# Performance work log

Hardware: AMD Instinct MI355X
Metric: run time of the kernel (lower is better)

## Reference

```python
import math
import jax, jax.numpy as jnp
import numpy as np

B, S, HID = 2, 2048, 3072
NH, HD = 32, 96            # num_heads, head_dim; num_kv_heads == num_heads (n_rep = 1)
OP = NH * HD + 2 * (NH * HD)  # 9216


def _rope_tables(seq_len, head_dim, theta=10000.0):
    inv_freq = 1.0 / (theta ** (np.arange(0, head_dim, 2, dtype=np.float32) / head_dim))
    t = np.arange(seq_len, dtype=np.float32)
    freqs = np.outer(t, inv_freq)                      # [S, HD/2]
    emb = np.concatenate([freqs, freqs], axis=-1)      # [S, HD]
    return jnp.asarray(np.cos(emb)), jnp.asarray(np.sin(emb))


def setup_inputs() -> dict:
    key = jax.random.key(0)
    k1, k2, k3 = jax.random.split(key, 3)
    hidden_states = jax.random.normal(k1, (B, S, HID), dtype=jnp.float32)
    cos, sin = _rope_tables(S, HD)
    # additive causal mask [B, 1, S, S]
    neg = jnp.finfo(jnp.float32).min
    causal = jnp.where(jnp.tril(jnp.ones((S, S), dtype=bool)), 0.0, neg)
    attention_mask = jnp.broadcast_to(causal[None, None], (B, 1, S, S)).astype(jnp.float32)
    Wqkv = jax.random.normal(k2, (HID, OP), dtype=jnp.float32) * (HID ** -0.5)
    Wo = jax.random.normal(k3, (NH * HD, HID), dtype=jnp.float32) * ((NH * HD) ** -0.5)
    return {"hidden_states": hidden_states, "cos": cos, "sin": sin,
            "attention_mask": attention_mask, "Wqkv": Wqkv, "Wo": Wo}


def _rotate_half(x):
    x1, x2 = jnp.split(x, 2, axis=-1)
    return jnp.concatenate([-x2, x1], axis=-1)


def reference(hidden_states, cos, sin, attention_mask, Wqkv, Wo):
    bsz, q_len, _ = hidden_states.shape
    qkv = hidden_states @ Wqkv                                    # [B,S,OP]
    q, k, v = jnp.split(qkv, [NH * HD, 2 * NH * HD], axis=-1)
    # [B,S,H*D] -> [B,H,S,D]
    to_bhsd = lambda t: t.reshape(bsz, q_len, NH, HD).transpose(0, 2, 1, 3)
    q, k, v = to_bhsd(q), to_bhsd(k), to_bhsd(v)
    c = cos[None, None]                                           # [1,1,S,D]
    s = sin[None, None]
    q = q * c + _rotate_half(q) * s
    k = k * c + _rotate_half(k) * s
    # num_key_value_groups == 1, so repeat_kv is identity.
    scores = jnp.einsum('bhqd,bhkd->bhqk', q, k) / math.sqrt(HD)  # [B,H,S,S]
    scores = scores + attention_mask
    attn = jax.nn.softmax(scores.astype(jnp.float32), axis=-1).astype(v.dtype)
    # dropout p=0.0 / eval -> identity
    out = jnp.einsum('bhqk,bhkd->bhqd', attn, v)                  # [B,H,S,D]
    out = out.transpose(0, 2, 1, 3).reshape(bsz, q_len, NH * HD)
    return out @ Wo                                               # [B,S,HID]
```

## Files before the change

kernel.cpp:

```cpp
#include <hip/hip_runtime.h>

typedef __bf16  bf16x8 __attribute__((ext_vector_type(8)));
typedef float   f32x4  __attribute__((ext_vector_type(4)));
typedef float   f32x16 __attribute__((ext_vector_type(16)));
typedef short   i16x8  __attribute__((ext_vector_type(8)));
typedef unsigned short u16x4 __attribute__((ext_vector_type(4)));
typedef unsigned int   u32x4 __attribute__((ext_vector_type(4)));

__device__ __forceinline__ float bf2f(unsigned short u) {
    union { unsigned int i; float f; } v; v.i = ((unsigned int)u) << 16; return v.f;
}
__device__ __forceinline__ unsigned short f2bf(float f) {
    union { float f; unsigned int i; } v; v.f = f;
    unsigned int r = v.i + 0x7FFFu + ((v.i >> 16) & 1u);
    return (unsigned short)(r >> 16);
}
__device__ __forceinline__ unsigned pk2(float lo, float hi) {
    union { __bf16 h[2]; unsigned u; } t;
    t.h[0] = (__bf16)lo; t.h[1] = (__bf16)hi;
    return t.u;
}
__device__ __forceinline__ unsigned short cvt1(float x) {
    union { __bf16 h; unsigned short u; } t;
    t.h = (__bf16)x;
    return t.u;
}
__device__ __forceinline__ void gload_lds16(const void* g, void* l) {
    __builtin_amdgcn_global_load_lds(
        (const __attribute__((address_space(1))) void*)g,
        (__attribute__((address_space(3))) void*)l, 16, 0, 0);
}
__device__ __forceinline__ void pswap(unsigned &x, unsigned &y) {
#if __has_builtin(__builtin_amdgcn_permlane32_swap)
    auto r = __builtin_amdgcn_permlane32_swap((int)x, (int)y, false, false);
    x = (unsigned)r[0]; y = (unsigned)r[1];
#else
    unsigned nx = (threadIdx.x & 32) ? (unsigned)__shfl_xor((int)y, 32) : x;
    unsigned ny = (threadIdx.x & 32) ? y : (unsigned)__shfl_xor((int)x, 32);
    x = nx; y = ny;
#endif
}
__device__ __forceinline__ float partner_f(float v, int hi) {
    unsigned x = __builtin_bit_cast(unsigned, v), y = x;
    pswap(x, y);
    return __builtin_bit_cast(float, hi ? x : y);
}

__global__ __launch_bounds__(256) void cast_f32_bf16(
    const float* __restrict__ in, unsigned short* __restrict__ out, int n8)
{
    int i = blockIdx.x * 256 + threadIdx.x;
    if (i >= n8) return;
    const f32x4* p = (const f32x4*)(in + (long)i * 8);
    f32x4 a = p[0], b = p[1];
    i16x8 o;
    o[0]=(short)f2bf(a[0]); o[1]=(short)f2bf(a[1]); o[2]=(short)f2bf(a[2]); o[3]=(short)f2bf(a[3]);
    o[4]=(short)f2bf(b[0]); o[5]=(short)f2bf(b[1]); o[6]=(short)f2bf(b[2]); o[7]=(short)f2bf(b[3]);
    *(i16x8*)(out + (long)i * 8) = o;
}

__global__ __launch_bounds__(256) void transpose_cast(
    const float* __restrict__ in, unsigned short* __restrict__ out, int R, int C)
{
    __shared__ float tile[64][65];
    int c0 = blockIdx.x * 64, r0 = blockIdx.y * 64;
    int tx = threadIdx.x & 63, ty = threadIdx.x >> 6;
#pragma unroll
    for (int i = 0; i < 64; i += 4)
        tile[ty + i][tx] = in[(long)(r0 + ty + i) * C + c0 + tx];
    __syncthreads();
#pragma unroll
    for (int i = 0; i < 64; i += 4)
        out[(long)(c0 + ty + i) * R + r0 + tx] = f2bf(tile[tx][ty + i]);
}

template <int MODE>
__global__ __launch_bounds__(256) void gemm_bt(
    const unsigned short* __restrict__ A, const unsigned short* __restrict__ B,
    int K, int N,
    unsigned short* __restrict__ Qo, unsigned short* __restrict__ Ko,
    unsigned short* __restrict__ Vo, float* __restrict__ Cf)
{
    __shared__ unsigned short Al[128 * 64];
    __shared__ unsigned short Bl[128 * 64];
    const int t = threadIdx.x;
    const int w = t >> 6, l = t & 63, lhi = l >> 4, llo = l & 15;
    const int m0 = blockIdx.x * 128, n0 = blockIdx.y * 128;
    const int wmo = (w >> 1) << 6, wno = (w & 1) << 6;

    const unsigned short* ag[4];
    const unsigned short* bg[4];
#pragma unroll
    for (int i = 0; i < 4; ++i) {
        int j = i * 256 + t;
        int row = j >> 3;
        int c = (j & 7) ^ (row & 7);
        ag[i] = A + (long)(m0 + row) * K + c * 8;
        bg[i] = B + (long)(n0 + row) * K + c * 8;
    }

    f32x4 acc[4][4] = {};
    const int nkt = K >> 6;
    for (int kt = 0; kt < nkt; ++kt) {
        __syncthreads();
#pragma unroll
        for (int i = 0; i < 4; ++i) {
            gload_lds16(ag[i] + kt * 64, &Al[(i * 256 + (w << 6)) * 8]);
            gload_lds16(bg[i] + kt * 64, &Bl[(i * 256 + (w << 6)) * 8]);
        }
        __syncthreads();
#pragma unroll
        for (int kf = 0; kf < 2; ++kf) {
            bf16x8 af[4], bfv[4];
#pragma unroll
            for (int mi = 0; mi < 4; ++mi) {
                int row = wmo + mi * 16 + llo;
                int cc = (kf * 4 + lhi) ^ (row & 7);
                af[mi] = __builtin_bit_cast(bf16x8, *(const i16x8*)&Al[row * 64 + cc * 8]);
            }
#pragma unroll
            for (int ni = 0; ni < 4; ++ni) {
                int row = wno + ni * 16 + llo;
                int cc = (kf * 4 + lhi) ^ (row & 7);
                bfv[ni] = __builtin_bit_cast(bf16x8, *(const i16x8*)&Bl[row * 64 + cc * 8]);
            }
#pragma unroll
            for (int mi = 0; mi < 4; ++mi)
#pragma unroll
                for (int ni = 0; ni < 4; ++ni)
                    acc[mi][ni] = __builtin_amdgcn_mfma_f32_16x16x32_bf16(
                        af[mi], bfv[ni], acc[mi][ni], 0, 0, 0);
        }
    }

#pragma unroll
    for (int mi = 0; mi < 4; ++mi) {
        int s0g = m0 + wmo + mi * 16 + (lhi << 2);
#pragma unroll
        for (int ni = 0; ni < 4; ++ni) {
            int gcol = n0 + wno + ni * 16 + llo;
            if (MODE == 1) {
#pragma unroll
                for (int r = 0; r < 4; ++r)
                    Cf[(long)(s0g + r) * N + gcol] = acc[mi][ni][r];
            } else {
                int seg = gcol / 3072;
                int cc2 = gcol - seg * 3072;
                int h = cc2 / 96, d = cc2 - h * 96;
                int b = s0g >> 11, s = s0g & 2047;
                long bh = (long)((b << 5) + h);
                if (seg == 2) {
                    u16x4 pv;
#pragma unroll
                    for (int r = 0; r < 4; ++r) pv[r] = f2bf(acc[mi][ni][r]);
                    *(u16x4*)(Vo + (bh * 96 + d) * 2048 + s) = pv;
                } else {
                    unsigned short* dst = seg ? Ko : Qo;
#pragma unroll
                    for (int r = 0; r < 4; ++r)
                        dst[(bh * 2048 + s + r) * 96 + d] = f2bf(acc[mi][ni][r]);
                }
            }
        }
    }
}

__global__ __launch_bounds__(256) void rope_kernel(
    unsigned short* __restrict__ Qb, unsigned short* __restrict__ Kb,
    const float* __restrict__ cosT, const float* __restrict__ sinT)
{
    int i = blockIdx.x * 256 + threadIdx.x;
    int d6 = i % 6;
    int sbh = i / 6;
    int s = sbh & 2047;
    long base = (long)sbh * 96 + d6 * 8;
    const f32x4* cp = (const f32x4*)(cosT + s * 96 + d6 * 8);
    const f32x4* sp = (const f32x4*)(sinT + s * 96 + d6 * 8);
    f32x4 c0 = cp[0], c1 = cp[1], s0 = sp[0], s1 = sp[1];
    float cv[8] = {c0[0],c0[1],c0[2],c0[3],c1[0],c1[1],c1[2],c1[3]};
    float sv[8] = {s0[0],s0[1],s0[2],s0[3],s1[0],s1[1],s1[2],s1[3]};
    i16x8 qlo = *(i16x8*)(Qb + base), qhi = *(i16x8*)(Qb + base + 48);
    i16x8 klo = *(i16x8*)(Kb + base), khi = *(i16x8*)(Kb + base + 48);
    i16x8 qlo2, qhi2, klo2, khi2;
#pragma unroll
    for (int j = 0; j < 8; ++j) {
        float ql = bf2f((unsigned short)qlo[j]), qh = bf2f((unsigned short)qhi[j]);
        float kl = bf2f((unsigned short)klo[j]), kh = bf2f((unsigned short)khi[j]);
        qlo2[j] = (short)f2bf(ql * cv[j] - qh * sv[j]);
        qhi2[j] = (short)f2bf(qh * cv[j] + ql * sv[j]);
        klo2[j] = (short)f2bf(kl * cv[j] - kh * sv[j]);
        khi2[j] = (short)f2bf(kh * cv[j] + kl * sv[j]);
    }
    *(i16x8*)(Qb + base) = qlo2; *(i16x8*)(Qb + base + 48) = qhi2;
    *(i16x8*)(Kb + base) = klo2; *(i16x8*)(Kb + base + 48) = khi2;
}

__global__ __launch_bounds__(256, 2) void attn_fwd(
    const unsigned short* __restrict__ Q, const unsigned short* __restrict__ Kt,
    const unsigned short* __restrict__ Vg, unsigned short* __restrict__ O)
{
    __shared__ __align__(16) unsigned short Kl[2][64 * 128];
    __shared__ __align__(16) unsigned short Vl[2][96 * 64];
    const int t = threadIdx.x;
    const int w = t >> 6, l = t & 63;
    const int l31 = l & 31, hi = l >> 5, l7 = l & 7;
    const int bh = blockIdx.x;
    constexpr float C2 = 0.14724450f;

    const unsigned short* Kg  = Kt + (long)bh * 2048 * 96;
    const unsigned short* Vgb = Vg + (long)bh * 96 * 2048;

#define STAGE_KV(buf, tile)                                                        \
    {                                                                              \
        _Pragma("unroll")                                                          \
        for (int i_ = 0; i_ < 4; ++i_) {                                           \
            int row_ = (w << 4) + (i_ << 2) + (l >> 4);                            \
            gload_lds16(Kg + ((long)(tile) * 64 + row_) * 96 +                     \
                            (((l & 15) ^ (row_ & 7)) << 3),                        \
                        &Kl[buf][((w << 4) + (i_ << 2)) << 7]);                    \
        }                                                                          \
        _Pragma("unroll")                                                          \
        for (int i_ = 0; i_ < 3; ++i_) {                                           \
            int row_ = w * 24 + (i_ << 3) + (l >> 3);                              \
            gload_lds16(Vgb + (long)row_ * 2048 + (tile) * 64 +                    \
                            ((l7 ^ (row_ & 7)) << 3),                              \
                        &Vl[buf][(w * 24 + (i_ << 3)) << 6]);                      \
        }                                                                          \
    }

    const int b = bh >> 5, h = bh & 31;

    for (int pass = 0; pass < 2; ++pass) {
        const int qt = pass ? 15 - (int)blockIdx.y : (int)blockIdx.y;
        const int q0b = qt << 7;
        const int nkv = 2 * qt + 2;
        const int kd  = 2 * qt + (w >> 1);

        bf16x8 qf[6];
        {
            const unsigned short* qp =
                Q + ((long)bh * 2048 + q0b + (w << 5) + l31) * 96 + (hi << 3);
#pragma unroll
            for (int ks = 0; ks < 6; ++ks)
                qf[ks] = __builtin_bit_cast(bf16x8, *(const i16x8*)(qp + ks * 16));
        }

        f32x16 oa[3] = {};
        float m_r = -1e30f, l_r = 0.f;

        STAGE_KV(0, 0);
        STAGE_KV(1, 1);

        for (int kt = 0; kt < nkv; ++kt) {
            const int cb = kt & 1;
            if (kt < nkv - 1) asm volatile("s_waitcnt vmcnt(7)" ::: "memory");
            else              asm volatile("s_waitcnt vmcnt(0)" ::: "memory");
            __builtin_amdgcn_s_barrier();

            if (kt <= kd) {
                f32x16 s0 = {}, s1 = {};
                __builtin_amdgcn_s_setprio(1);
#pragma unroll
                for (int ks = 0; ks < 6; ++ks) {
                    bf16x8 k0 = __builtin_bit_cast(bf16x8, *(const i16x8*)
                        &Kl[cb][(l31 << 7) + ((((ks << 1) + hi) ^ l7) << 3)]);
                    bf16x8 k1 = __builtin_bit_cast(bf16x8, *(const i16x8*)
                        &Kl[cb][((32 + l31) << 7) + ((((ks << 1) + hi) ^ l7) << 3)]);
                    s0 = __builtin_amdgcn_mfma_f32_32x32x16_bf16(k0, qf[ks], s0, 0, 0, 0);
                    s1 = __builtin_amdgcn_mfma_f32_32x32x16_bf16(k1, qf[ks], s1, 0, 0, 0);
                }
                __builtin_amdgcn_s_setprio(0);

                if (kt == kd) {
#pragma unroll
                    for (int r = 0; r < 16; ++r) {
                        int kvl = (r & 3) + ((r >> 2) << 3) + (hi << 2);
                        if (w & 1) {
                            if (kvl > l31) s1[r] = -1e30f;
                        } else {
                            if (kvl > l31) s0[r] = -1e30f;
                            s1[r] = -1e30f;
                        }
                    }
                }
                float px = s0[0];
#pragma unroll
                for (int r = 1; r < 16; ++r) px = fmaxf(px, s0[r]);
#pragma unroll
                for (int r = 0; r < 16; ++r) px = fmaxf(px, s1[r]);
                px = fmaxf(px, partner_f(px, hi));
                if (__any(px > m_r + 54.0f)) {
                    float mnew = fmaxf(m_r, px);
                    float scl = exp2f((m_r - mnew) * C2);
                    l_r *= scl;
#pragma unroll
                    for (int tt = 0; tt < 3; ++tt)
#pragma unroll
                        for (int r = 0; r < 16; ++r) oa[tt][r] *= scl;
                    m_r = mnew;
                }
                const float mC = m_r * C2;
                float ls = 0.f;
#pragma unroll
                for (int r = 0; r < 16; ++r) {
                    s0[r] = exp2f(fmaf(s0[r], C2, -mC));
                    s1[r] = exp2f(fmaf(s1[r], C2, -mC));
                    ls += s0[r] + s1[r];
                }
                l_r += ls;
                bf16x8 pf[4];
#pragma unroll
                for (int s = 0; s < 4; ++s) {
                    const f32x16& pv = (s >= 2) ? s1 : s0;
                    const int bb = (s & 1) << 3;
                    unsigned d0 = pk2(pv[bb + 0], pv[bb + 1]);
                    unsigned d2 = pk2(pv[bb + 4], pv[bb + 5]);
                    pswap(d0, d2);
                    unsigned d1 = pk2(pv[bb + 2], pv[bb + 3]);
                    unsigned d3 = pk2(pv[bb + 6], pv[bb + 7]);
                    pswap(d1, d3);
                    pf[s] = __builtin_bit_cast(bf16x8, (u32x4){d0, d1, d2, d3});
                }
                __builtin_amdgcn_s_setprio(1);
#pragma unroll
                for (int s = 0; s < 4; ++s) {
#pragma unroll
                    for (int tt = 0; tt < 3; ++tt) {
                        bf16x8 vf = __builtin_bit_cast(bf16x8, *(const i16x8*)
                            &Vl[cb][((tt << 5) + l31) * 64 + ((((s << 1) + hi) ^ l7) << 3)]);
                        oa[tt] = __builtin_amdgcn_mfma_f32_32x32x16_bf16(vf, pf[s], oa[tt], 0, 0, 0);
                    }
                }
                __builtin_amdgcn_s_setprio(0);
            }

            asm volatile("s_waitcnt lgkmcnt(0)" ::: "memory");
            __builtin_amdgcn_s_barrier();
            if (kt + 2 < nkv) STAGE_KV(cb, kt + 2);
        }

        {
            float lt = l_r + partner_f(l_r, hi);
            float inv = 1.0f / lt;
            const int qg = q0b + (w << 5) + l31;
            unsigned short* ob = O + ((long)(b * 2048 + qg)) * 3072 + h * 96;
#pragma unroll
            for (int tt = 0; tt < 3; ++tt)
#pragma unroll
                for (int qd = 0; qd < 4; ++qd) {
                    u16x4 o4;
#pragma unroll
                    for (int j = 0; j < 4; ++j)
                        o4[j] = cvt1(oa[tt][(qd << 2) + j] * inv);
                    *(u16x4*)(ob + (tt << 5) + (qd << 3) + (hi << 2)) = o4;
                }
        }
    }
#undef STAGE_KV
}

extern "C" void kernel_launch(void* const* d_in, const int* in_sizes, int n_in,
                              void* d_out, int out_size, void* d_ws, size_t ws_size,
                              hipStream_t stream) {
    const float* hidden = (const float*)d_in[0];
    const float* cosT   = (const float*)d_in[1];
    const float* sinT   = (const float*)d_in[2];
    const float* Wqkv   = (const float*)d_in[4];
    const float* Wo     = (const float*)d_in[5];
    float* out = (float*)d_out;

    char* ws = (char*)d_ws;
    unsigned short* Ah  = (unsigned short*)ws;
    unsigned short* WqT = (unsigned short*)(ws + 25165824);
    unsigned short* Qb  = (unsigned short*)(ws + 25165824 + 56623104);
    unsigned short* Kb  = Qb + 12582912;
    unsigned short* Vb  = Kb + 12582912;

    cast_f32_bf16<<<6144, 256, 0, stream>>>(hidden, Ah, 1572864);
    transpose_cast<<<dim3(144, 48), 256, 0, stream>>>(Wqkv, WqT, 3072, 9216);
    gemm_bt<0><<<dim3(32, 72), 256, 0, stream>>>(Ah, WqT, 3072, 9216, Qb, Kb, Vb, nullptr);
    transpose_cast<<<dim3(48, 48), 256, 0, stream>>>(Wo, WqT, 3072, 3072);
    rope_kernel<<<3072, 256, 0, stream>>>(Qb, Kb, cosT, sinT);
    attn_fwd<<<dim3(64, 8), 256, 0, stream>>>(Qb, Kb, Vb, Ah);
    gemm_bt<1><<<dim3(32, 24), 256, 0, stream>>>(Ah, WqT, 3072, 3072,
                                                 nullptr, nullptr, nullptr, out);
}
```

Measured before the change: 513.6 us.

## Process paired causal query tiles together sharing one K/V stream

Instead of two sequential passes over K/V (one per query tile of the balanced pair), each block now holds both query tiles' fragments and accumulators and streams K/V once, applying each tile's step while the tile is still within its causal range. This removes the redundant re-staging of K/V for the shorter tile and halves the number of loop prologues and barriers. In exchange, register pressure roughly doubles for Q fragments and output accumulators, which under launch_bounds(256,2) risks spilling or reduced occupancy.

New measurement: 510.4 us (median of 3 runs). No clear change (-0.6%).

```diff
diff --git a/kernel.cpp b/kernel.cpp
--- a/kernel.cpp
+++ b/kernel.cpp
@@ -195,6 +195,88 @@
     *(i16x8*)(Kb + base) = klo2; *(i16x8*)(Kb + base + 48) = khi2;
 }
 
+__device__ __forceinline__ void attn_step(
+    const unsigned short* __restrict__ Kb, const unsigned short* __restrict__ Vb,
+    const bf16x8 (&qf)[6], f32x16 (&oa)[3], float &m_r, float &l_r,
+    const bool diag, const int w, const int l31, const int hi, const int l7)
+{
+    constexpr float C2 = 0.14724450f;
+    f32x16 s0 = {}, s1 = {};
+    __builtin_amdgcn_s_setprio(1);
+#pragma unroll
+    for (int ks = 0; ks < 6; ++ks) {
+        bf16x8 k0 = __builtin_bit_cast(bf16x8, *(const i16x8*)
+            &Kb[(l31 << 7) + ((((ks << 1) + hi) ^ l7) << 3)]);
+        bf16x8 k1 = __builtin_bit_cast(bf16x8, *(const i16x8*)
+            &Kb[((32 + l31) << 7) + ((((ks << 1) + hi) ^ l7) << 3)]);
+        s0 = __builtin_amdgcn_mfma_f32_32x32x16_bf16(k0, qf[ks], s0, 0, 0, 0);
+        s1 = __builtin_amdgcn_mfma_f32_32x32x16_bf16(k1, qf[ks], s1, 0, 0, 0);
+    }
+    __builtin_amdgcn_s_setprio(0);
+
+    if (diag) {
+#pragma unroll
+        for (int r = 0; r < 16; ++r) {
+            int kvl = (r & 3) + ((r >> 2) << 3) + (hi << 2);
+            if (w & 1) {
+                if (kvl > l31) s1[r] = -1e30f;
+            } else {
+                if (kvl > l31) s0[r] = -1e30f;
+                s1[r] = -1e30f;
+            }
+        }
+    }
+    float px = s0[0];
+#pragma unroll
+    for (int r = 1; r < 16; ++r) px = fmaxf(px, s0[r]);
+#pragma unroll
+    for (int r = 0; r < 16; ++r) px = fmaxf(px, s1[r]);
+    px = fmaxf(px, partner_f(px, hi));
+    if (__any(px > m_r + 54.0f)) {
+        float mnew = fmaxf(m_r, px);
+        float scl = exp2f((m_r - mnew) * C2);
+        l_r *= scl;
+#pragma unroll
+        for (int tt = 0; tt < 3; ++tt)
+#pragma unroll
+            for (int r = 0; r < 16; ++r) oa[tt][r] *= scl;
+        m_r = mnew;
+    }
+    const float mC = m_r * C2;
+    float ls = 0.f;
+#pragma unroll
+    for (int r = 0; r < 16; ++r) {
+        s0[r] = exp2f(fmaf(s0[r], C2, -mC));
+        s1[r] = exp2f(fmaf(s1[r], C2, -mC));
+        ls += s0[r] + s1[r];
+    }
+    l_r += ls;
+    bf16x8 pf[4];
+#pragma unroll
+    for (int s = 0; s < 4; ++s) {
+        const f32x16& pv = (s >= 2) ? s1 : s0;
+        const int bb = (s & 1) << 3;
+        unsigned d0 = pk2(pv[bb + 0], pv[bb + 1]);
+        unsigned d2 = pk2(pv[bb + 4], pv[bb + 5]);
+        pswap(d0, d2);
+        unsigned d1 = pk2(pv[bb + 2], pv[bb + 3]);
+        unsigned d3 = pk2(pv[bb + 6], pv[bb + 7]);
+        pswap(d1, d3);
+        pf[s] = __builtin_bit_cast(bf16x8, (u32x4){d0, d1, d2, d3});
+    }
+    __builtin_amdgcn_s_setprio(1);
+#pragma unroll
+    for (int s = 0; s < 4; ++s) {
+#pragma unroll
+        for (int tt = 0; tt < 3; ++tt) {
+            bf16x8 vf = __builtin_bit_cast(bf16x8, *(const i16x8*)
+                &Vb[((tt << 5) + l31) * 64 + ((((s << 1) + hi) ^ l7) << 3)]);
+            oa[tt] = __builtin_amdgcn_mfma_f32_32x32x16_bf16(vf, pf[s], oa[tt], 0, 0, 0);
+        }
+    }
+    __builtin_amdgcn_s_setprio(0);
+}
+
 __global__ __launch_bounds__(256, 2) void attn_fwd(
     const unsigned short* __restrict__ Q, const unsigned short* __restrict__ Kt,
     const unsigned short* __restrict__ Vg, unsigned short* __restrict__ O)
@@ -205,7 +287,6 @@
     const int w = t >> 6, l = t & 63;
     const int l31 = l & 31, hi = l >> 5, l7 = l & 7;
     const int bh = blockIdx.x;
-    constexpr float C2 = 0.14724450f;
 
     const unsigned short* Kg  = Kt + (long)bh * 2048 * 96;
     const unsigned short* Vgb = Vg + (long)bh * 96 * 2048;
@@ -229,134 +310,68 @@
     }
 
     const int b = bh >> 5, h = bh & 31;
-
-    for (int pass = 0; pass < 2; ++pass) {
-        const int qt = pass ? 15 - (int)blockIdx.y : (int)blockIdx.y;
-        const int q0b = qt << 7;
-        const int nkv = 2 * qt + 2;
-        const int kd  = 2 * qt + (w >> 1);
-
-        bf16x8 qf[6];
-        {
-            const unsigned short* qp =
-                Q + ((long)bh * 2048 + q0b + (w << 5) + l31) * 96 + (hi << 3);
-#pragma unroll
-            for (int ks = 0; ks < 6; ++ks)
-                qf[ks] = __builtin_bit_cast(bf16x8, *(const i16x8*)(qp + ks * 16));
-        }
-
-        f32x16 oa[3] = {};
-        float m_r = -1e30f, l_r = 0.f;
-
-        STAGE_KV(0, 0);
-        STAGE_KV(1, 1);
-
-        for (int kt = 0; kt < nkv; ++kt) {
-            const int cb = kt & 1;
-            if (kt < nkv - 1) asm volatile("s_waitcnt vmcnt(7)" ::: "memory");
-            else              asm volatile("s_waitcnt vmcnt(0)" ::: "memory");
-            __builtin_amdgcn_s_barrier();
-
-            if (kt <= kd) {
-                f32x16 s0 = {}, s1 = {};
-                __builtin_amdgcn_s_setprio(1);
-#pragma unroll
-                for (int ks = 0; ks < 6; ++ks) {
-                    bf16x8 k0 = __builtin_bit_cast(bf16x8, *(const i16x8*)
-                        &Kl[cb][(l31 << 7) + ((((ks << 1) + hi) ^ l7) << 3)]);
-                    bf16x8 k1 = __builtin_bit_cast(bf16x8, *(const i16x8*)
-                        &Kl[cb][((32 + l31) << 7) + ((((ks << 1) + hi) ^ l7) << 3)]);
-                    s0 = __builtin_amdgcn_mfma_f32_32x32x16_bf16(k0, qf[ks], s0, 0, 0, 0);
-                    s1 = __builtin_amdgcn_mfma_f32_32x32x16_bf16(k1, qf[ks], s1, 0, 0, 0);
-                }
-                __builtin_amdgcn_s_setprio(0);
-
-                if (kt == kd) {
-#pragma unroll
-                    for (int r = 0; r < 16; ++r) {
-                        int kvl = (r & 3) + ((r >> 2) << 3) + (hi << 2);
-                        if (w & 1) {
-                            if (kvl > l31) s1[r] = -1e30f;
-                        } else {
-                            if (kvl > l31) s0[r] = -1e30f;
-                            s1[r] = -1e30f;
-                        }
-                    }
-                }
-                float px = s0[0];
-#pragma unroll
-                for (int r = 1; r < 16; ++r) px = fmaxf(px, s0[r]);
-#pragma unroll
-                for (int r = 0; r < 16; ++r) px = fmaxf(px, s1[r]);
-                px = fmaxf(px, partner_f(px, hi));
-                if (__any(px > m_r + 54.0f)) {
-                    float mnew = fmaxf(m_r, px);
-                    float scl = exp2f((m_r - mnew) * C2);
-                    l_r *= scl;
-#pragma unroll
-                    for (int tt = 0; tt < 3; ++tt)
-#pragma unroll
-                        for (int r = 0; r < 16; ++r) oa[tt][r] *= scl;
-                    m_r = mnew;
-                }
-                const float mC = m_r * C2;
-                float ls = 0.f;
-#pragma unroll
-                for (int r = 0; r < 16; ++r) {
-                    s0[r] = exp2f(fmaf(s0[r], C2, -mC));
-                    s1[r] = exp2f(fmaf(s1[r], C2, -mC));
-                    ls += s0[r] + s1[r];
-                }
-                l_r += ls;
-                bf16x8 pf[4];
-#pragma unroll
-                for (int s = 0; s < 4; ++s) {
-                    const f32x16& pv = (s >= 2) ? s1 : s0;
-                    const int bb = (s & 1) << 3;
-                    unsigned d0 = pk2(pv[bb + 0], pv[bb + 1]);
-                    unsigned d2 = pk2(pv[bb + 4], pv[bb + 5]);
-                    pswap(d0, d2);
-                    unsigned d1 = pk2(pv[bb + 2], pv[bb + 3]);
-                    unsigned d3 = pk2(pv[bb + 6], pv[bb + 7]);
-                    pswap(d1, d3);
-                    pf[s] = __builtin_bit_cast(bf16x8, (u32x4){d0, d1, d2, d3});
-                }
-                __builtin_amdgcn_s_setprio(1);
-#pragma unroll
-                for (int s = 0; s < 4; ++s) {
-#pragma unroll
-                    for (int tt = 0; tt < 3; ++tt) {
-                        bf16x8 vf = __builtin_bit_cast(bf16x8, *(const i16x8*)
-                            &Vl[cb][((tt << 5) + l31) * 64 + ((((s << 1) + hi) ^ l7) << 3)]);
-                        oa[tt] = __builtin_amdgcn_mfma_f32_32x32x16_bf16(vf, pf[s], oa[tt], 0, 0, 0);
-                    }
-                }
-                __builtin_amdgcn_s_setprio(0);
+    const int qtA = (int)blockIdx.y, qtB = 15 - qtA;
+    const int q0A = qtA << 7, q0B = qtB << 7;
+    const int nkv = 2 * qtB + 2;
+    const int kdA = 2 * qtA + (w >> 1);
+    const int kdB = 2 * qtB + (w >> 1);
+
+    bf16x8 qfA[6], qfB[6];
+    {
+        const unsigned short* qpA =
+            Q + ((long)bh * 2048 + q0A + (w << 5) + l31) * 96 + (hi << 3);
+        const unsigned short* qpB =
+            Q + ((long)bh * 2048 + q0B + (w << 5) + l31) * 96 + (hi << 3);
+#pragma unroll
+        for (int ks = 0; ks < 6; ++ks) {
+            qfA[ks] = __builtin_bit_cast(bf16x8, *(const i16x8*)(qpA + ks * 16));
+            qfB[ks] = __builtin_bit_cast(bf16x8, *(const i16x8*)(qpB + ks * 16));
+        }
+    }
+
+    f32x16 oaA[3] = {}, oaB[3] = {};
+    float mA = -1e30f, lA = 0.f, mB = -1e30f, lB = 0.f;
+
+    STAGE_KV(0, 0);
+    STAGE_KV(1, 1);
+
+    for (int kt = 0; kt < nkv; ++kt) {
+        const int cb = kt & 1;
+        if (kt < nkv - 1) asm volatile("s_waitcnt vmcnt(7)" ::: "memory");
+        else              asm volatile("s_waitcnt vmcnt(0)" ::: "memory");
+        __builtin_amdgcn_s_barrier();
+
+        if (kt <= kdA)
+            attn_step(Kl[cb], Vl[cb], qfA, oaA, mA, lA, kt == kdA, w, l31, hi, l7);
+        if (kt <= kdB)
+            attn_step(Kl[cb], Vl[cb], qfB, oaB, mB, lB, kt == kdB, w, l31, hi, l7);
+
+        asm volatile("s_waitcnt lgkmcnt(0)" ::: "memory");
+        __builtin_amdgcn_s_barrier();
+        if (kt + 2 < nkv) STAGE_KV(cb, kt + 2);
+    }
+#undef STAGE_KV
+
+#pragma unroll
+    for (int which = 0; which < 2; ++which) {
+        const f32x16* oa = which ? oaB : oaA;
+        float l_r = which ? lB : lA;
+        const int q0b = which ? q0B : q0A;
+        float lt = l_r + partner_f(l_r, hi);
+        float inv = 1.0f / lt;
+        const int qg = q0b + (w << 5) + l31;
+        unsigned short* ob = O + ((long)(b * 2048 + qg)) * 3072 + h * 96;
+#pragma unroll
+        for (int tt = 0; tt < 3; ++tt)
+#pragma unroll
+            for (int qd = 0; qd < 4; ++qd) {
+                u16x4 o4;
+#pragma unroll
+                for (int j = 0; j < 4; ++j)
+                    o4[j] = cvt1(oa[tt][(qd << 2) + j] * inv);
+                *(u16x4*)(ob + (tt << 5) + (qd << 3) + (hi << 2)) = o4;
             }
-
-            asm volatile("s_waitcnt lgkmcnt(0)" ::: "memory");
-            __builtin_amdgcn_s_barrier();
-            if (kt + 2 < nkv) STAGE_KV(cb, kt + 2);
-        }
-
-        {
-            float lt = l_r + partner_f(l_r, hi);
-            float inv = 1.0f / lt;
-            const int qg = q0b + (w << 5) + l31;
-            unsigned short* ob = O + ((long)(b * 2048 + qg)) * 3072 + h * 96;
-#pragma unroll
-            for (int tt = 0; tt < 3; ++tt)
-#pragma unroll
-                for (int qd = 0; qd < 4; ++qd) {
-                    u16x4 o4;
-#pragma unroll
-                    for (int j = 0; j < 4; ++j)
-                        o4[j] = cvt1(oa[tt][(qd << 2) + j] * inv);
-                    *(u16x4*)(ob + (tt << 5) + (qd << 3) + (hi << 2)) = o4;
-                }
-        }
-    }
-#undef STAGE_KV
+    }
 }
 
 extern "C" void kernel_launch(void* const* d_in, const int* in_sizes, int n_in,
```
